# Performance work log

Hardware: AMD Instinct MI355X
Metric: run time of the kernel (lower is better)

The kernel has to match this reference:

```python
import jax, jax.numpy as jnp
import numpy as np
import math

N_NODES = 50000
N_EDGES = 1600000
DIM = 64
HEADS = 8
EDGE_DIM = 32


def setup_inputs() -> dict:
    key = jax.random.key(0)
    ks = jax.random.split(key, 12)
    s = 1.0 / math.sqrt(DIM)
    se = 1.0 / math.sqrt(EDGE_DIM)
    return {
        'x': jax.random.normal(ks[0], (N_NODES, DIM), jnp.float32),
        'edge_index': jax.random.randint(ks[1], (2, N_EDGES), 0, N_NODES),
        'edge_attr': jax.random.normal(ks[2], (N_EDGES, EDGE_DIM), jnp.float32),
        'WQ': jax.random.normal(ks[3], (DIM, DIM), jnp.float32) * s,
        'bQ': jnp.zeros((DIM,), jnp.float32),
        'WK': jax.random.normal(ks[4], (DIM, DIM), jnp.float32) * s,
        'bK': jnp.zeros((DIM,), jnp.float32),
        'WV': jax.random.normal(ks[5], (DIM, DIM), jnp.float32) * s,
        'bV': jnp.zeros((DIM,), jnp.float32),
        'WO': jax.random.normal(ks[6], (DIM, DIM), jnp.float32) * s,
        'bO': jnp.zeros((DIM,), jnp.float32),
        'We1': jax.random.normal(ks[7], (EDGE_DIM, EDGE_DIM), jnp.float32) * se,
        'be1': jnp.zeros((EDGE_DIM,), jnp.float32),
        'We2': jax.random.normal(ks[8], (EDGE_DIM, HEADS), jnp.float32) * se,
        'be2': jnp.zeros((HEADS,), jnp.float32),
    }


def graph_softmax(src, index, num_segments):
    # src: [E, H], index: [E] -> per-destination-node stable softmax
    smax = jax.ops.segment_max(src, index, num_segments=num_segments)  # [N, H]
    smax = jnp.where(jnp.isfinite(smax), smax, 0.0)  # nodes with no edges
    e = jnp.exp(src - smax[index])
    ssum = jax.ops.segment_sum(e, index, num_segments=num_segments) + 1e-12
    return e / ssum[index]


def reference(x, edge_index, edge_attr, WQ, bQ, WK, bK, WV, bV, WO, bO, We1, be1, We2, be2):
    num_nodes = x.shape[0]
    d_k = DIM // HEADS
    i, j = edge_index[0], edge_index[1]
    # per-node projections [N, H, d_k], then gather per-edge
    Q = (x @ WQ + bQ).reshape(num_nodes, HEADS, d_k)
    K = (x @ WK + bK).reshape(num_nodes, HEADS, d_k)
    V = (x @ WV + bV).reshape(num_nodes, HEADS, d_k)
    query = Q[j]  # [E, H, d_k]
    key = K[i]
    value = V[i]
    # edge bias MLP: [edge_dim -> edge_dim -> num_heads] with SiLU between
    h = jax.nn.silu(edge_attr @ We1 + be1)
    bias = h @ We2 + be2  # [E, H]
    scores = jnp.sum(query * key, axis=-1) / math.sqrt(d_k) + bias  # [E, H]
    alpha = graph_softmax(scores, j, num_nodes)  # [E, H]
    weighted = (alpha[..., None] * value).reshape(-1, DIM)  # [E, dim]
    attn_out = jax.ops.segment_sum(weighted, j, num_segments=num_nodes)  # [N, dim]
    return attn_out @ WO + bO
```

## Files before the change

### kernel.cpp

```cpp
#include <hip/hip_runtime.h>
#include <math.h>

#define N_NODES 50000
#define N_EDGES 1600000
#define DIM 64
#define HEADS 8
#define EDGE_DIM 32

#define NB 256
#define NPB 196
#define ACAP 8192
#define PART_T 512
#define EPT 4
#define PART_E (PART_T * EPT)

typedef __fp16 h2 __attribute__((ext_vector_type(2)));

__device__ __forceinline__ unsigned int f2bf(float f) {
    union { float f; unsigned int u; } c; c.f = f;
    unsigned int u = c.u;
    return (u + 0x7FFFu + ((u >> 16) & 1u)) >> 16;
}
__device__ __forceinline__ float bf_lo(unsigned int u) { return __uint_as_float(u << 16); }
__device__ __forceinline__ float bf_hi(unsigned int u) { return __uint_as_float(u & 0xFFFF0000u); }

__global__ __launch_bounds__(1024) void pack_weights(
    const float* __restrict__ We1, const float* __restrict__ We2,
    h2* __restrict__ w1p, h2* __restrict__ w2p)
{
    const int t = threadIdx.x;
    if (t < 512) {
        const int c = t >> 4, kk = t & 15;
        w1p[t] = __builtin_amdgcn_cvt_pkrtz(We1[(2 * kk) * EDGE_DIM + c],
                                            We1[(2 * kk + 1) * EDGE_DIM + c]);
    } else if (t < 512 + 128) {
        const int u = t - 512;
        const int h = u >> 4, cc = u & 15;
        w2p[u] = __builtin_amdgcn_cvt_pkrtz(We2[(2 * cc) * HEADS + h],
                                            We2[(2 * cc + 1) * HEADS + h]);
    }
}

__global__ __launch_bounds__(512) void mlp_partition(
    const int* __restrict__ ei,
    const float* __restrict__ edge_attr,
    const h2* __restrict__ w1p, const float* __restrict__ be1,
    const h2* __restrict__ w2p, const float* __restrict__ be2,
    int* __restrict__ gcur,
    uint2* __restrict__ A_rec, uint4* __restrict__ bias_by_e)
{
    __shared__ int cnt[NB];
    __shared__ int base[NB];
    __shared__ int lbase[NB];
    __shared__ int total_s;
    __shared__ uint2 srec[PART_E];
    __shared__ unsigned char sbkt[PART_E];
    const int tid = threadIdx.x;
    if (tid < NB) cnt[tid] = 0;
    __syncthreads();
    const int e0 = blockIdx.x * PART_E;
    #pragma unroll
    for (int k = 0; k < EPT; ++k) {
        const int e = e0 + k * PART_T + tid;
        if (e < N_EDGES) atomicAdd(&cnt[ei[N_EDGES + e] / NPB], 1);
    }
    __syncthreads();
    if (tid < NB) lbase[tid] = cnt[tid];
    __syncthreads();
    for (int o = 1; o < NB; o <<= 1) {
        int t = 0;
        if (tid < NB && tid >= o) t = lbase[tid - o];
        __syncthreads();
        if (tid < NB) lbase[tid] += t;
        __syncthreads();
    }
    if (tid < NB) {
        const int inc = lbase[tid];
        const int c = cnt[tid];
        base[tid] = (c > 0) ? atomicAdd(&gcur[tid], c) : 0;
        lbase[tid] = inc - c;
        if (tid == NB - 1) total_s = inc;
        cnt[tid] = 0;
    }
    __syncthreads();
    for (int k = 0; k < EPT; ++k) {
        const int e = e0 + k * PART_T + tid;
        if (e >= N_EDGES) break;
        const int i = ei[e];
        const int j = ei[N_EDGES + e];
        const int b = j / NPB;
        const int jl = j - b * NPB;
        float a[EDGE_DIM];
        const float4* ar = (const float4*)(edge_attr + (size_t)e * EDGE_DIM);
        #pragma unroll
        for (int q = 0; q < EDGE_DIM / 4; ++q) {
            float4 v = ar[q];
            a[q * 4 + 0] = v.x; a[q * 4 + 1] = v.y;
            a[q * 4 + 2] = v.z; a[q * 4 + 3] = v.w;
        }
        h2 a2[EDGE_DIM / 2];
        #pragma unroll
        for (int kk = 0; kk < EDGE_DIM / 2; ++kk)
            a2[kk] = __builtin_amdgcn_cvt_pkrtz(a[2 * kk], a[2 * kk + 1]);
        float sil[EDGE_DIM];
        #pragma unroll 8
        for (int c = 0; c < EDGE_DIM; ++c) {
            float s = be1[c];
            #pragma unroll
            for (int kk = 0; kk < EDGE_DIM / 2; ++kk)
                s = __builtin_amdgcn_fdot2(a2[kk], w1p[c * 16 + kk], s, false);
            sil[c] = __fdividef(s, 1.0f + __expf(-s));
        }
        h2 s2[EDGE_DIM / 2];
        #pragma unroll
        for (int cc = 0; cc < EDGE_DIM / 2; ++cc)
            s2[cc] = __builtin_amdgcn_cvt_pkrtz(sil[2 * cc], sil[2 * cc + 1]);
        float b0f = be2[0], b1f = be2[1], b2f = be2[2], b3f = be2[3];
        float b4f = be2[4], b5f = be2[5], b6f = be2[6], b7f = be2[7];
        #pragma unroll
        for (int cc = 0; cc < EDGE_DIM / 2; ++cc) {
            b0f = __builtin_amdgcn_fdot2(s2[cc], w2p[0 * 16 + cc], b0f, false);
            b1f = __builtin_amdgcn_fdot2(s2[cc], w2p[1 * 16 + cc], b1f, false);
            b2f = __builtin_amdgcn_fdot2(s2[cc], w2p[2 * 16 + cc], b2f, false);
            b3f = __builtin_amdgcn_fdot2(s2[cc], w2p[3 * 16 + cc], b3f, false);
            b4f = __builtin_amdgcn_fdot2(s2[cc], w2p[4 * 16 + cc], b4f, false);
            b5f = __builtin_amdgcn_fdot2(s2[cc], w2p[5 * 16 + cc], b5f, false);
            b6f = __builtin_amdgcn_fdot2(s2[cc], w2p[6 * 16 + cc], b6f, false);
            b7f = __builtin_amdgcn_fdot2(s2[cc], w2p[7 * 16 + cc], b7f, false);
        }
        uint4 br;
        br.x = f2bf(b0f) | (f2bf(b1f) << 16);
        br.y = f2bf(b2f) | (f2bf(b3f) << 16);
        br.z = f2bf(b4f) | (f2bf(b5f) << 16);
        br.w = f2bf(b6f) | (f2bf(b7f) << 16);
        bias_by_e[e] = br;
        const int s = lbase[b] + atomicAdd(&cnt[b], 1);
        srec[s] = make_uint2((unsigned)e, ((unsigned)jl << 24) | (unsigned)i);
        sbkt[s] = (unsigned char)b;
    }
    __syncthreads();
    const int total = total_s;
    for (int s = tid; s < total; s += PART_T) {
        const int b = sbkt[s];
        const int gp = base[b] + (s - lbase[b]);
        if (gp < ACAP) A_rec[(size_t)b * ACAP + gp] = srec[s];
    }
}

__global__ __launch_bounds__(512) void bucket_perm(
    const int* __restrict__ gcur,
    const uint2* __restrict__ A_rec,
    int* __restrict__ offs, uint2* __restrict__ es_sorted)
{
    __shared__ int sc[NB];
    __shared__ int ldeg[NPB];
    __shared__ int loff[NPB + 1];
    __shared__ int gbase_s;
    const int tid = threadIdx.x;
    const int b = blockIdx.x;
    if (tid < NB) sc[tid] = min(gcur[tid], ACAP);
    __syncthreads();
    for (int o = 1; o < NB; o <<= 1) {
        int t = 0;
        if (tid < NB && tid >= o) t = sc[tid - o];
        __syncthreads();
        if (tid < NB) sc[tid] += t;
        __syncthreads();
    }
    if (tid == 0) gbase_s = (b == 0) ? 0 : sc[b - 1];
    if (tid < NPB) ldeg[tid] = 0;
    __syncthreads();
    const int gbase = gbase_s;
    const int nb = min(gcur[b], ACAP);
    for (int r = tid; r < nb; r += 512)
        atomicAdd(&ldeg[A_rec[(size_t)b * ACAP + r].y >> 24], 1);
    __syncthreads();
    if (tid < 256) sc[tid] = (tid < NPB) ? ldeg[tid] : 0;
    __syncthreads();
    for (int o = 1; o < 256; o <<= 1) {
        int t = 0;
        if (tid < 256 && tid >= o) t = sc[tid - o];
        __syncthreads();
        if (tid < 256) sc[tid] += t;
        __syncthreads();
    }
    if (tid == 0) loff[0] = 0;
    if (tid < NPB) { loff[tid + 1] = sc[tid]; ldeg[tid] = 0; }
    __syncthreads();
    const int jbase = b * NPB;
    if (tid < NPB && jbase + tid < N_NODES) offs[jbase + tid] = gbase + loff[tid];
    if (b == NB - 1 && tid == 0) offs[N_NODES] = gbase + nb;
    for (int r = tid; r < nb; r += 512) {
        const uint2 rec = A_rec[(size_t)b * ACAP + r];
        const int jl = (int)(rec.y >> 24);
        const int slot = loff[jl] + atomicAdd(&ldeg[jl], 1);
        es_sorted[(size_t)gbase + slot] = make_uint2(rec.x, rec.y & 0xFFFFFFu);
    }
}

__global__ __launch_bounds__(256) void qkv_proj(
    const float* __restrict__ x,
    const float* __restrict__ WQ, const float* __restrict__ bQ,
    const float* __restrict__ WK, const float* __restrict__ bK,
    const float* __restrict__ WV, const float* __restrict__ bV,
    float* __restrict__ Q, unsigned int* __restrict__ KV)
{
    __shared__ float sWQ[DIM * DIM];
    __shared__ float sWK[DIM * DIM];
    __shared__ float sWV[DIM * DIM];
    for (int t = threadIdx.x; t < DIM * DIM; t += blockDim.x) {
        sWQ[t] = WQ[t]; sWK[t] = WK[t]; sWV[t] = WV[t];
    }
    __syncthreads();
    const int lane = threadIdx.x & 63;
    const int wave = threadIdx.x >> 6;
    const int n = blockIdx.x * 4 + wave;
    if (n >= N_NODES) return;
    float xl = x[(size_t)n * DIM + lane];
    float aq = bQ[lane], ak = bK[lane], av = bV[lane];
    #pragma unroll
    for (int k = 0; k < DIM; ++k) {
        float xv = __shfl(xl, k, 64);
        aq += xv * sWQ[k * DIM + lane];
        ak += xv * sWK[k * DIM + lane];
        av += xv * sWV[k * DIM + lane];
    }
    Q[(size_t)n * DIM + lane] = aq;
    KV[(size_t)n * DIM + lane] = f2bf(ak) | (f2bf(av) << 16);
}

__global__ __launch_bounds__(256) void node_attn_out(
    const int* __restrict__ off,
    const uint2* __restrict__ es_sorted,
    const unsigned short* __restrict__ bias_u16,
    const float* __restrict__ Q, const unsigned int* __restrict__ KV,
    const float* __restrict__ WO, const float* __restrict__ bO,
    float* __restrict__ out)
{
    __shared__ float sWO[DIM * DIM];
    for (int t = threadIdx.x; t < DIM * DIM; t += 256) sWO[t] = WO[t];
    __syncthreads();
    const int lane = threadIdx.x & 63;
    const int wave = threadIdx.x >> 6;
    const int j = blockIdx.x * 4 + wave;
    if (j >= N_NODES) return;
    const int beg = off[j], end = off[j + 1];
    const int h = lane >> 3;
    const float qv = Q[(size_t)j * DIM + lane];
    const float inv_sqrt_dk = 0.35355339059327373f;
    float num = 0.0f;
    float den = 1e-12f;
    int t = beg;
    for (; t + 3 < end; t += 4) {
        const uint2 r0 = es_sorted[t + 0];
        const uint2 r1 = es_sorted[t + 1];
        const uint2 r2 = es_sorted[t + 2];
        const uint2 r3 = es_sorted[t + 3];
        const unsigned int u0 = KV[(size_t)r0.y * DIM + lane];
        const unsigned int u1 = KV[(size_t)r1.y * DIM + lane];
        const unsigned int u2 = KV[(size_t)r2.y * DIM + lane];
        const unsigned int u3 = KV[(size_t)r3.y * DIM + lane];
        const float b0 = bf_lo((unsigned int)bias_u16[(size_t)r0.x * HEADS + h]);
        const float b1 = bf_lo((unsigned int)bias_u16[(size_t)r1.x * HEADS + h]);
        const float b2 = bf_lo((unsigned int)bias_u16[(size_t)r2.x * HEADS + h]);
        const float b3 = bf_lo((unsigned int)bias_u16[(size_t)r3.x * HEADS + h]);
        float d0 = qv * bf_lo(u0);
        float d1 = qv * bf_lo(u1);
        float d2 = qv * bf_lo(u2);
        float d3 = qv * bf_lo(u3);
        d0 += __shfl_xor(d0, 1, 64); d1 += __shfl_xor(d1, 1, 64);
        d2 += __shfl_xor(d2, 1, 64); d3 += __shfl_xor(d3, 1, 64);
        d0 += __shfl_xor(d0, 2, 64); d1 += __shfl_xor(d1, 2, 64);
        d2 += __shfl_xor(d2, 2, 64); d3 += __shfl_xor(d3, 2, 64);
        d0 += __shfl_xor(d0, 4, 64); d1 += __shfl_xor(d1, 4, 64);
        d2 += __shfl_xor(d2, 4, 64); d3 += __shfl_xor(d3, 4, 64);
        const float e0 = __expf(d0 * inv_sqrt_dk + b0);
        const float e1 = __expf(d1 * inv_sqrt_dk + b1);
        const float e2 = __expf(d2 * inv_sqrt_dk + b2);
        const float e3 = __expf(d3 * inv_sqrt_dk + b3);
        num += e0 * bf_hi(u0) + e1 * bf_hi(u1) + e2 * bf_hi(u2) + e3 * bf_hi(u3);
        den += e0 + e1 + e2 + e3;
    }
    for (; t < end; ++t) {
        const uint2 r0 = es_sorted[t];
        const unsigned int u0 = KV[(size_t)r0.y * DIM + lane];
        const float b0 = bf_lo((unsigned int)bias_u16[(size_t)r0.x * HEADS + h]);
        float d0 = qv * bf_lo(u0);
        d0 += __shfl_xor(d0, 1, 64);
        d0 += __shfl_xor(d0, 2, 64);
        d0 += __shfl_xor(d0, 4, 64);
        const float e0 = __expf(d0 * inv_sqrt_dk + b0);
        num += e0 * bf_hi(u0);
        den += e0;
    }
    const float av = num / den;
    float acc = bO[lane];
    #pragma unroll
    for (int k = 0; k < DIM; ++k) {
        acc += __shfl(av, k, 64) * sWO[k * DIM + lane];
    }
    out[(size_t)j * DIM + lane] = acc;
}

extern "C" void kernel_launch(void* const* d_in, const int* in_sizes, int n_in,
                              void* d_out, int out_size, void* d_ws, size_t ws_size,
                              hipStream_t stream) {
    const float* x    = (const float*)d_in[0];
    const int*   ei   = (const int*)d_in[1];
    const float* ea   = (const float*)d_in[2];
    const float* WQ   = (const float*)d_in[3];
    const float* bQ   = (const float*)d_in[4];
    const float* WK   = (const float*)d_in[5];
    const float* bK   = (const float*)d_in[6];
    const float* WV   = (const float*)d_in[7];
    const float* bV   = (const float*)d_in[8];
    const float* WO   = (const float*)d_in[9];
    const float* bO   = (const float*)d_in[10];
    const float* We1  = (const float*)d_in[11];
    const float* be1  = (const float*)d_in[12];
    const float* We2  = (const float*)d_in[13];
    const float* be2  = (const float*)d_in[14];
    float* out = (float*)d_out;

    char* ws = (char*)d_ws;
    size_t off_b = 0;
    auto alloc = [&](size_t bytes) {
        void* p = ws + off_b;
        off_b += (bytes + 255) & ~(size_t)255;
        return p;
    };
    float*        Q         = (float*)alloc((size_t)N_NODES * DIM * sizeof(float));
    unsigned int* KV        = (unsigned int*)alloc((size_t)N_NODES * DIM * sizeof(unsigned int));
    uint2*        A_rec     = (uint2*)alloc((size_t)NB * ACAP * sizeof(uint2));
    uint4*        bias_by_e = (uint4*)alloc((size_t)N_EDGES * sizeof(uint4));
    uint2*        es_sorted = (uint2*)alloc((size_t)N_EDGES * sizeof(uint2));
    int*          offs      = (int*)alloc((size_t)(N_NODES + 1) * sizeof(int));
    int*          gcur      = (int*)alloc((size_t)NB * sizeof(int));
    h2*           w1p       = (h2*)alloc(512 * sizeof(h2));
    h2*           w2p       = (h2*)alloc(128 * sizeof(h2));

    (void)hipMemsetAsync(gcur, 0, (size_t)NB * sizeof(int), stream);

    pack_weights<<<1, 1024, 0, stream>>>(We1, We2, w1p, w2p);
    mlp_partition<<<(N_EDGES + PART_E - 1) / PART_E, PART_T, 0, stream>>>(
        ei, ea, w1p, be1, w2p, be2, gcur, A_rec, bias_by_e);
    bucket_perm<<<NB, 512, 0, stream>>>(gcur, A_rec, offs, es_sorted);
    qkv_proj<<<(N_NODES + 3) / 4, 256, 0, stream>>>(x, WQ, bQ, WK, bK, WV, bV, Q, KV);
    node_attn_out<<<(N_NODES + 3) / 4, 256, 0, stream>>>(offs, es_sorted,
                                                         (const unsigned short*)bias_by_e,
                                                         Q, KV, WO, bO, out);
}
```

Before: 349.0 us.

## Merge bucket permutation with QKV projection and deepen gather unroll

Merges the bucket_perm and qkv_proj kernels into one launch, with the first NB blocks doing the per-bucket permutation and the remaining blocks doing the QKV projection. The two independent stages can then overlap on the GPU and one launch is saved. The memset of gcur is folded into pack_weights, and mlp_partition drops to 256 threads per block so its predicates go away. The node attention loop gets an 8-edge unrolled path that issues more gathers in flight, at the cost of higher register pressure.

```diff
diff --git a/kernel.cpp b/kernel.cpp
--- a/kernel.cpp
+++ b/kernel.cpp
@@ -10,9 +10,11 @@
 #define NB 256
 #define NPB 196
 #define ACAP 8192
-#define PART_T 512
+#define PART_T 256
 #define EPT 4
 #define PART_E (PART_T * EPT)
+
+#define QKV_BLKS 12500
 
 typedef __fp16 h2 __attribute__((ext_vector_type(2)));
 
@@ -26,7 +28,7 @@
 
 __global__ __launch_bounds__(1024) void pack_weights(
     const float* __restrict__ We1, const float* __restrict__ We2,
-    h2* __restrict__ w1p, h2* __restrict__ w2p)
+    h2* __restrict__ w1p, h2* __restrict__ w2p, int* __restrict__ gcur)
 {
     const int t = threadIdx.x;
     if (t < 512) {
@@ -38,10 +40,12 @@
         const int h = u >> 4, cc = u & 15;
         w2p[u] = __builtin_amdgcn_cvt_pkrtz(We2[(2 * cc) * HEADS + h],
                                             We2[(2 * cc + 1) * HEADS + h]);
-    }
-}
-
-__global__ __launch_bounds__(512) void mlp_partition(
+    } else if (t >= 768 && t < 768 + NB) {
+        gcur[t - 768] = 0;
+    }
+}
+
+__global__ __launch_bounds__(256) void mlp_partition(
     const int* __restrict__ ei,
     const float* __restrict__ edge_attr,
     const h2* __restrict__ w1p, const float* __restrict__ be1,
@@ -56,7 +60,7 @@
     __shared__ uint2 srec[PART_E];
     __shared__ unsigned char sbkt[PART_E];
     const int tid = threadIdx.x;
-    if (tid < NB) cnt[tid] = 0;
+    cnt[tid] = 0;
     __syncthreads();
     const int e0 = blockIdx.x * PART_E;
     #pragma unroll
@@ -65,16 +69,15 @@
         if (e < N_EDGES) atomicAdd(&cnt[ei[N_EDGES + e] / NPB], 1);
     }
     __syncthreads();
-    if (tid < NB) lbase[tid] = cnt[tid];
+    lbase[tid] = cnt[tid];
     __syncthreads();
     for (int o = 1; o < NB; o <<= 1) {
-        int t = 0;
-        if (tid < NB && tid >= o) t = lbase[tid - o];
-        __syncthreads();
-        if (tid < NB) lbase[tid] += t;
-        __syncthreads();
-    }
-    if (tid < NB) {
+        int t = (tid >= o) ? lbase[tid - o] : 0;
+        __syncthreads();
+        lbase[tid] += t;
+        __syncthreads();
+    }
+    {
         const int inc = lbase[tid];
         const int c = cnt[tid];
         base[tid] = (c > 0) ? atomicAdd(&gcur[tid], c) : 0;
@@ -147,86 +150,83 @@
     }
 }
 
-__global__ __launch_bounds__(512) void bucket_perm(
-    const int* __restrict__ gcur,
-    const uint2* __restrict__ A_rec,
-    int* __restrict__ offs, uint2* __restrict__ es_sorted)
-{
-    __shared__ int sc[NB];
-    __shared__ int ldeg[NPB];
-    __shared__ int loff[NPB + 1];
-    __shared__ int gbase_s;
-    const int tid = threadIdx.x;
-    const int b = blockIdx.x;
-    if (tid < NB) sc[tid] = min(gcur[tid], ACAP);
-    __syncthreads();
-    for (int o = 1; o < NB; o <<= 1) {
-        int t = 0;
-        if (tid < NB && tid >= o) t = sc[tid - o];
-        __syncthreads();
-        if (tid < NB) sc[tid] += t;
-        __syncthreads();
-    }
-    if (tid == 0) gbase_s = (b == 0) ? 0 : sc[b - 1];
-    if (tid < NPB) ldeg[tid] = 0;
-    __syncthreads();
-    const int gbase = gbase_s;
-    const int nb = min(gcur[b], ACAP);
-    for (int r = tid; r < nb; r += 512)
-        atomicAdd(&ldeg[A_rec[(size_t)b * ACAP + r].y >> 24], 1);
-    __syncthreads();
-    if (tid < 256) sc[tid] = (tid < NPB) ? ldeg[tid] : 0;
-    __syncthreads();
-    for (int o = 1; o < 256; o <<= 1) {
-        int t = 0;
-        if (tid < 256 && tid >= o) t = sc[tid - o];
-        __syncthreads();
-        if (tid < 256) sc[tid] += t;
-        __syncthreads();
-    }
-    if (tid == 0) loff[0] = 0;
-    if (tid < NPB) { loff[tid + 1] = sc[tid]; ldeg[tid] = 0; }
-    __syncthreads();
-    const int jbase = b * NPB;
-    if (tid < NPB && jbase + tid < N_NODES) offs[jbase + tid] = gbase + loff[tid];
-    if (b == NB - 1 && tid == 0) offs[N_NODES] = gbase + nb;
-    for (int r = tid; r < nb; r += 512) {
-        const uint2 rec = A_rec[(size_t)b * ACAP + r];
-        const int jl = (int)(rec.y >> 24);
-        const int slot = loff[jl] + atomicAdd(&ldeg[jl], 1);
-        es_sorted[(size_t)gbase + slot] = make_uint2(rec.x, rec.y & 0xFFFFFFu);
-    }
-}
-
-__global__ __launch_bounds__(256) void qkv_proj(
+__global__ __launch_bounds__(256) void perm_qkv(
+    const int* __restrict__ gcur, const uint2* __restrict__ A_rec,
+    int* __restrict__ offs, uint2* __restrict__ es_sorted,
     const float* __restrict__ x,
     const float* __restrict__ WQ, const float* __restrict__ bQ,
     const float* __restrict__ WK, const float* __restrict__ bK,
     const float* __restrict__ WV, const float* __restrict__ bV,
     float* __restrict__ Q, unsigned int* __restrict__ KV)
 {
-    __shared__ float sWQ[DIM * DIM];
-    __shared__ float sWK[DIM * DIM];
-    __shared__ float sWV[DIM * DIM];
-    for (int t = threadIdx.x; t < DIM * DIM; t += blockDim.x) {
-        sWQ[t] = WQ[t]; sWK[t] = WK[t]; sWV[t] = WV[t];
-    }
-    __syncthreads();
-    const int lane = threadIdx.x & 63;
-    const int wave = threadIdx.x >> 6;
-    const int n = blockIdx.x * 4 + wave;
-    if (n >= N_NODES) return;
-    float xl = x[(size_t)n * DIM + lane];
-    float aq = bQ[lane], ak = bK[lane], av = bV[lane];
-    #pragma unroll
-    for (int k = 0; k < DIM; ++k) {
-        float xv = __shfl(xl, k, 64);
-        aq += xv * sWQ[k * DIM + lane];
-        ak += xv * sWK[k * DIM + lane];
-        av += xv * sWV[k * DIM + lane];
-    }
-    Q[(size_t)n * DIM + lane] = aq;
-    KV[(size_t)n * DIM + lane] = f2bf(ak) | (f2bf(av) << 16);
+    __shared__ __align__(16) char smem[3 * DIM * DIM * sizeof(float)];
+    const int tid = threadIdx.x;
+    if (blockIdx.x < NB) {
+        int* sc   = (int*)smem;
+        int* ldeg = sc + NB;
+        int* loff = ldeg + NPB;
+        int* gb   = loff + NPB + 1;
+        const int b = blockIdx.x;
+        sc[tid] = min(gcur[tid], ACAP);
+        __syncthreads();
+        for (int o = 1; o < NB; o <<= 1) {
+            int t = (tid >= o) ? sc[tid - o] : 0;
+            __syncthreads();
+            sc[tid] += t;
+            __syncthreads();
+        }
+        if (tid == 0) gb[0] = (b == 0) ? 0 : sc[b - 1];
+        if (tid < NPB) ldeg[tid] = 0;
+        __syncthreads();
+        const int gbase = gb[0];
+        const int nb = min(gcur[b], ACAP);
+        for (int r = tid; r < nb; r += 256)
+            atomicAdd(&ldeg[A_rec[(size_t)b * ACAP + r].y >> 24], 1);
+        __syncthreads();
+        sc[tid] = (tid < NPB) ? ldeg[tid] : 0;
+        __syncthreads();
+        for (int o = 1; o < 256; o <<= 1) {
+            int t = (tid >= o) ? sc[tid - o] : 0;
+            __syncthreads();
+            sc[tid] += t;
+            __syncthreads();
+        }
+        if (tid == 0) loff[0] = 0;
+        if (tid < NPB) { loff[tid + 1] = sc[tid]; ldeg[tid] = 0; }
+        __syncthreads();
+        const int jbase = b * NPB;
+        if (tid < NPB && jbase + tid < N_NODES) offs[jbase + tid] = gbase + loff[tid];
+        if (b == NB - 1 && tid == 0) offs[N_NODES] = gbase + nb;
+        for (int r = tid; r < nb; r += 256) {
+            const uint2 rec = A_rec[(size_t)b * ACAP + r];
+            const int jl = (int)(rec.y >> 24);
+            const int slot = loff[jl] + atomicAdd(&ldeg[jl], 1);
+            es_sorted[(size_t)gbase + slot] = make_uint2(rec.x, rec.y & 0xFFFFFFu);
+        }
+    } else {
+        float* sWQ = (float*)smem;
+        float* sWK = sWQ + DIM * DIM;
+        float* sWV = sWK + DIM * DIM;
+        for (int t = tid; t < DIM * DIM; t += 256) {
+            sWQ[t] = WQ[t]; sWK[t] = WK[t]; sWV[t] = WV[t];
+        }
+        __syncthreads();
+        const int lane = tid & 63;
+        const int wave = tid >> 6;
+        const int n = (blockIdx.x - NB) * 4 + wave;
+        if (n >= N_NODES) return;
+        float xl = x[(size_t)n * DIM + lane];
+        float aq = bQ[lane], ak = bK[lane], av = bV[lane];
+        #pragma unroll
+        for (int k = 0; k < DIM; ++k) {
+            float xv = __shfl(xl, k, 64);
+            aq += xv * sWQ[k * DIM + lane];
+            ak += xv * sWK[k * DIM + lane];
+            av += xv * sWV[k * DIM + lane];
+        }
+        Q[(size_t)n * DIM + lane] = aq;
+        KV[(size_t)n * DIM + lane] = f2bf(ak) | (f2bf(av) << 16);
+    }
 }
 
 __global__ __launch_bounds__(256) void node_attn_out(
@@ -251,35 +251,57 @@
     float num = 0.0f;
     float den = 1e-12f;
     int t = beg;
+    for (; t + 7 < end; t += 8) {
+        uint2 r[8];
+        unsigned int u[8];
+        float bb[8], d[8];
+        #pragma unroll
+        for (int q = 0; q < 8; ++q) r[q] = es_sorted[t + q];
+        #pragma unroll
+        for (int q = 0; q < 8; ++q) u[q] = KV[(size_t)r[q].y * DIM + lane];
+        #pragma unroll
+        for (int q = 0; q < 8; ++q)
+            bb[q] = bf_lo((unsigned int)bias_u16[(size_t)r[q].x * HEADS + h]);
+        #pragma unroll
+        for (int q = 0; q < 8; ++q) d[q] = qv * bf_lo(u[q]);
+        #pragma unroll
+        for (int q = 0; q < 8; ++q) d[q] += __shfl_xor(d[q], 1, 64);
+        #pragma unroll
+        for (int q = 0; q < 8; ++q) d[q] += __shfl_xor(d[q], 2, 64);
+        #pragma unroll
+        for (int q = 0; q < 8; ++q) d[q] += __shfl_xor(d[q], 4, 64);
+        #pragma unroll
+        for (int q = 0; q < 8; ++q) {
+            const float ev = __expf(d[q] * inv_sqrt_dk + bb[q]);
+            num += ev * bf_hi(u[q]);
+            den += ev;
+        }
+    }
     for (; t + 3 < end; t += 4) {
-        const uint2 r0 = es_sorted[t + 0];
-        const uint2 r1 = es_sorted[t + 1];
-        const uint2 r2 = es_sorted[t + 2];
-        const uint2 r3 = es_sorted[t + 3];
-        const unsigned int u0 = KV[(size_t)r0.y * DIM + lane];
-        const unsigned int u1 = KV[(size_t)r1.y * DIM + lane];
-        const unsigned int u2 = KV[(size_t)r2.y * DIM + lane];
-        const unsigned int u3 = KV[(size_t)r3.y * DIM + lane];
-        const float b0 = bf_lo((unsigned int)bias_u16[(size_t)r0.x * HEADS + h]);
-        const float b1 = bf_lo((unsigned int)bias_u16[(size_t)r1.x * HEADS + h]);
-        const float b2 = bf_lo((unsigned int)bias_u16[(size_t)r2.x * HEADS + h]);
-        const float b3 = bf_lo((unsigned int)bias_u16[(size_t)r3.x * HEADS + h]);
-        float d0 = qv * bf_lo(u0);
-        float d1 = qv * bf_lo(u1);
-        float d2 = qv * bf_lo(u2);
-        float d3 = qv * bf_lo(u3);
-        d0 += __shfl_xor(d0, 1, 64); d1 += __shfl_xor(d1, 1, 64);
-        d2 += __shfl_xor(d2, 1, 64); d3 += __shfl_xor(d3, 1, 64);
-        d0 += __shfl_xor(d0, 2, 64); d1 += __shfl_xor(d1, 2, 64);
-        d2 += __shfl_xor(d2, 2, 64); d3 += __shfl_xor(d3, 2, 64);
-        d0 += __shfl_xor(d0, 4, 64); d1 += __shfl_xor(d1, 4, 64);
-        d2 += __shfl_xor(d2, 4, 64); d3 += __shfl_xor(d3, 4, 64);
-        const float e0 = __expf(d0 * inv_sqrt_dk + b0);
-        const float e1 = __expf(d1 * inv_sqrt_dk + b1);
-        const float e2 = __expf(d2 * inv_sqrt_dk + b2);
-        const float e3 = __expf(d3 * inv_sqrt_dk + b3);
-        num += e0 * bf_hi(u0) + e1 * bf_hi(u1) + e2 * bf_hi(u2) + e3 * bf_hi(u3);
-        den += e0 + e1 + e2 + e3;
+        uint2 r[4];
+        unsigned int u[4];
+        float bb[4], d[4];
+        #pragma unroll
+        for (int q = 0; q < 4; ++q) r[q] = es_sorted[t + q];
+        #pragma unroll
+        for (int q = 0; q < 4; ++q) u[q] = KV[(size_t)r[q].y * DIM + lane];
+        #pragma unroll
+        for (int q = 0; q < 4; ++q)
+            bb[q] = bf_lo((unsigned int)bias_u16[(size_t)r[q].x * HEADS + h]);
+        #pragma unroll
+        for (int q = 0; q < 4; ++q) d[q] = qv * bf_lo(u[q]);
+        #pragma unroll
+        for (int q = 0; q < 4; ++q) d[q] += __shfl_xor(d[q], 1, 64);
+        #pragma unroll
+        for (int q = 0; q < 4; ++q) d[q] += __shfl_xor(d[q], 2, 64);
+        #pragma unroll
+        for (int q = 0; q < 4; ++q) d[q] += __shfl_xor(d[q], 4, 64);
+        #pragma unroll
+        for (int q = 0; q < 4; ++q) {
+            const float ev = __expf(d[q] * inv_sqrt_dk + bb[q]);
+            num += ev * bf_hi(u[q]);
+            den += ev;
+        }
     }
     for (; t < end; ++t) {
         const uint2 r0 = es_sorted[t];
@@ -339,13 +361,11 @@
     h2*           w1p       = (h2*)alloc(512 * sizeof(h2));
     h2*           w2p       = (h2*)alloc(128 * sizeof(h2));
 
-    (void)hipMemsetAsync(gcur, 0, (size_t)NB * sizeof(int), stream);
-
-    pack_weights<<<1, 1024, 0, stream>>>(We1, We2, w1p, w2p);
+    pack_weights<<<1, 1024, 0, stream>>>(We1, We2, w1p, w2p, gcur);
     mlp_partition<<<(N_EDGES + PART_E - 1) / PART_E, PART_T, 0, stream>>>(
         ei, ea, w1p, be1, w2p, be2, gcur, A_rec, bias_by_e);
-    bucket_perm<<<NB, 512, 0, stream>>>(gcur, A_rec, offs, es_sorted);
-    qkv_proj<<<(N_NODES + 3) / 4, 256, 0, stream>>>(x, WQ, bQ, WK, bK, WV, bV, Q, KV);
+    perm_qkv<<<NB + QKV_BLKS, 256, 0, stream>>>(gcur, A_rec, offs, es_sorted,
+                                                x, WQ, bQ, WK, bK, WV, bV, Q, KV);
     node_attn_out<<<(N_NODES + 3) / 4, 256, 0, stream>>>(offs, es_sorted,
                                                          (const unsigned short*)bias_by_e,
                                                          Q, KV, WO, bO, out);
```

New measurement: 325.4 us. 1.07x faster.
